# Kernel optimization log

Measured on AMD Instinct MI355X. Metric: run time of the kernel, lower is better.

Reference implementation:

```python
import jax, jax.numpy as jnp
import numpy as np

T, B, D = 512, 64, 1024


def setup_inputs() -> dict:
    key = jax.random.key(0)
    k1, k2, k3, k4 = jax.random.split(key, 4)
    scale = 1.0 / np.sqrt(D)
    x = jax.random.normal(k1, (T, B, D), dtype=jnp.float32)
    resets = jax.random.randint(k2, (T, B), 0, 2) > 0  # bool reset mask per step
    Wi = jax.random.normal(k3, (D, 3 * D), dtype=jnp.float32) * scale  # [ir|iz|in]
    bi = jnp.zeros((3 * D,), dtype=jnp.float32)
    Wh = jax.random.normal(k4, (D, 3 * D), dtype=jnp.float32) * scale  # [hr|hz|hn]
    bhn = jnp.zeros((D,), dtype=jnp.float32)  # bias only on hn gate (flax GRUCell)
    return {"x": x, "Wi": Wi, "bi": bi, "Wh": Wh, "bhn": bhn, "resets": resets}


def reference(x, Wi, bi, Wh, bhn, resets):
    """Scan of flax nn.GRUCell with reset-masked carry. x: [T,B,D], resets: [T,B] bool."""
    Bsz, Dh = x.shape[1], x.shape[2]

    def step(h, inp):
        xt, rt = inp  # xt: [B,D], rt: [B]
        h = jnp.where(rt[:, None], jnp.zeros_like(h), h)  # reset carry to zeros
        gi = xt @ Wi + bi          # [B,3D]
        gh = h @ Wh                # [B,3D] (no bias for r,z in flax GRUCell)
        ir_, iz_, in_ = jnp.split(gi, 3, axis=-1)
        hr_, hz_, hn_ = jnp.split(gh, 3, axis=-1)
        r = jax.nn.sigmoid(ir_ + hr_)
        z = jax.nn.sigmoid(iz_ + hz_)
        n = jnp.tanh(in_ + r * (hn_ + bhn))
        h_new = (1.0 - z) * n + z * h
        return h_new, h_new

    h0 = jnp.zeros((Bsz, Dh), dtype=x.dtype)  # flax initialize_carry default: zeros
    _, ys = jax.lax.scan(step, h0, (x, resets))
    return ys  # [T,B,D]
```

## Files before the change

### kernel.cpp

```cpp
#include <hip/hip_runtime.h>


typedef __attribute__((ext_vector_type(8))) short short8;
typedef __attribute__((ext_vector_type(4))) float f32x4;
typedef __attribute__((ext_vector_type(4))) unsigned int u32x4;

#define DEV static __device__ __forceinline__

constexpr int TT = 512, BB = 64, DD = 1024, TD = 3072;

constexpr size_t WS_BAR = 256;
constexpr size_t WS_H = 8192;
constexpr size_t HPLANE = (size_t)BB * DD * 2;
constexpr size_t WS_NEED = WS_H + 4 * HPLANE;

DEV unsigned short f2bf(float f) {
    unsigned u = __builtin_bit_cast(unsigned, f);
    u += 0x7FFFu + ((u >> 16) & 1u);
    return (unsigned short)(u >> 16);
}
DEV float bf2f(unsigned short s) { return __builtin_bit_cast(float, ((unsigned)s) << 16); }

DEV void ld16_sc1(u32x4& r, const unsigned* p) {
    asm volatile("global_load_dwordx4 %0, %1, off sc1" : "=v"(r) : "v"(p));
}
DEV void ld16(u32x4& r, const unsigned* p) {
    asm volatile("global_load_dwordx4 %0, %1, off" : "=v"(r) : "v"(p));
}
DEV void ld8u(unsigned& r, const unsigned char* p) {
    asm volatile("global_load_ubyte %0, %1, off" : "=v"(r) : "v"(p));
}
DEV void st16_sc1(unsigned short* p, unsigned v) {
    asm volatile("global_store_short %0, %1, off sc1" :: "v"(p), "v"(v) : "memory");
}
DEV void coh_store_u32(unsigned* p, unsigned v) {
    asm volatile("global_store_dword %0, %1, off sc1" :: "v"(p), "v"(v) : "memory");
}
DEV void vm0() {
    asm volatile("s_waitcnt vmcnt(0)" ::: "memory");
    __builtin_amdgcn_sched_barrier(0);
}

__global__ void pack_x_kernel(const float* __restrict__ x, unsigned* __restrict__ outw) {
    const size_t gid = (size_t)blockIdx.x * 256 + threadIdx.x;
    const size_t e0 = gid * 8;
    const unsigned t = (unsigned)(e0 >> 16);
    const unsigned p = (unsigned)(e0 & 65535u);
    f32x4 a = *(const f32x4*)(x + e0);
    f32x4 b = *(const f32x4*)(x + e0 + 4);
    u32x4 wh, wl;
#pragma unroll
    for (int j = 0; j < 2; ++j) {
        unsigned short h0 = f2bf(a[2 * j]), h1 = f2bf(a[2 * j + 1]);
        wh[j] = (unsigned)h0 | ((unsigned)h1 << 16);
        wl[j] = (unsigned)f2bf(a[2 * j] - bf2f(h0)) | ((unsigned)f2bf(a[2 * j + 1] - bf2f(h1)) << 16);
        unsigned short g0 = f2bf(b[2 * j]), g1 = f2bf(b[2 * j + 1]);
        wh[2 + j] = (unsigned)g0 | ((unsigned)g1 << 16);
        wl[2 + j] = (unsigned)f2bf(b[2 * j] - bf2f(g0)) | ((unsigned)f2bf(b[2 * j + 1] - bf2f(g1)) << 16);
    }
    unsigned* base = outw + (size_t)t * 65536u;
    *(u32x4*)(base + (p >> 1)) = wh;
    *(u32x4*)(base + 32768u + (p >> 1)) = wl;
}

__global__ void prep_kernel(const unsigned char* __restrict__ resets, unsigned char* __restrict__ ws) {
    const int bid = blockIdx.x, tid = threadIdx.x;
    if (bid < 256) {
        ((unsigned*)(ws + WS_H))[bid * 256 + tid] = 0u;
    } else {
        unsigned* w32 = (unsigned*)ws;
        for (int i = tid; i < 2048; i += 256) w32[i] = 0u;
        __shared__ int ca, cb, cc;
        if (tid == 0) { ca = 0; cb = 0; cc = 0; }
        __syncthreads();
        int la = 0, lb = 0, lc = 0;
        for (int o = tid * 16; o < tid * 16 + 16; ++o) {
            unsigned char v = resets[o];
            if (v) {
                if ((o & 3) == 0) la = 1; else lb = 1;
                if ((o & 7) == 4) lc = 1;
            }
        }
        if (la) atomicOr(&ca, 1);
        if (lb) atomicOr(&cb, 1);
        if (lc) atomicOr(&cc, 1);
        __syncthreads();
        if (tid == 0) {
            unsigned stride, boff = 0;
            if (ca && cb)       { stride = 1; }
            else if (!ca && cb) { stride = 4; boff = 3; }
            else if (ca && cc)  { stride = 4; }
            else if (ca)        { stride = 8; }
            else                { stride = 4; }
            w32[0] = stride; w32[1] = boff;
        }
    }
}

DEV void arrive_epoch(unsigned* bar, int grp, unsigned ep) {
    unsigned old = __hip_atomic_fetch_add(&bar[grp * 32], 1u, __ATOMIC_RELAXED, __HIP_MEMORY_SCOPE_AGENT);
    if (old == ep * 16u - 1u) {
        unsigned oldr = __hip_atomic_fetch_add(&bar[512], 1u, __ATOMIC_RELAXED, __HIP_MEMORY_SCOPE_AGENT);
        if (oldr == ep * 16u - 1u) {
#pragma unroll
            for (int g = 0; g < 16; ++g) coh_store_u32(&bar[544 + g * 32], ep);
            asm volatile("s_waitcnt vmcnt(0)" ::: "memory");
        }
    }
}
DEV void wait_epoch(unsigned* bar, int grp, unsigned ep) {
    while (__hip_atomic_load(&bar[544 + grp * 32], __ATOMIC_RELAXED, __HIP_MEMORY_SCOPE_AGENT) < ep) {}
}

__launch_bounds__(512, 1)
__global__ void gru_kernel(const float* __restrict__ Wi, const float* __restrict__ bi,
                           const float* __restrict__ Wh, const float* __restrict__ bhn,
                           const unsigned char* __restrict__ resets,
                           float* __restrict__ out, unsigned char* __restrict__ ws) {
    const int tid = threadIdx.x;
    const int wg = blockIdx.x;
    const int lane = tid & 63;
    const int kw = tid >> 6;
    const int mgrp = wg >> 6;
    const int c0 = (wg & 63) * 16;
    const int grp = wg >> 4;

    unsigned* bar = (unsigned*)(ws + WS_BAR);
    const unsigned rstride = ((const unsigned*)ws)[0];
    const unsigned rboff   = ((const unsigned*)ws)[1];

    unsigned short* h_hi[2] = {(unsigned short*)(ws + WS_H),
                               (unsigned short*)(ws + WS_H + 2 * HPLANE)};
    unsigned short* h_lo[2] = {(unsigned short*)(ws + WS_H + HPLANE),
                               (unsigned short*)(ws + WS_H + 3 * HPLANE)};
    unsigned* outw = (unsigned*)out;

    const int lrow = lane & 15;
    const int lk = (lane >> 4) * 8;

    short8 bih[3][4], bhh[3][4], bhl[3][4];
#pragma unroll
    for (int nt = 0; nt < 3; ++nt) {
        const int col = nt * DD + c0 + lrow;
#pragma unroll
        for (int kt = 0; kt < 4; ++kt) {
            const int kb = kw * 128 + kt * 32 + lk;
            short8 a, c, d;
#pragma unroll
            for (int j = 0; j < 8; ++j) {
                float wi = Wi[(size_t)(kb + j) * TD + col];
                a[j] = (short)f2bf(wi);
                float wh = Wh[(size_t)(kb + j) * TD + col];
                unsigned short h2 = f2bf(wh);
                c[j] = (short)h2;
                d[j] = (short)f2bf(wh - bf2f(h2));
            }
            bih[nt][kt] = a; bhh[nt][kt] = c; bhl[nt][kt] = d;
        }
    }

    const int eb = (tid & 255) >> 4, ej = tid & 15;
    const int brow = mgrp * 16 + eb;
    const int ce = c0 + ej;
    const float bi_r = bi[ce], bi_z = bi[DD + ce], bi_n = bi[2 * DD + ce];
    const float bh_n = bhn[ce];
    float h_local = 0.f;

    const int arow = mgrp * 16 + lrow;
    const unsigned hidx = (unsigned)(arow * DD + kw * 128 + lk);
    const size_t r64 = (size_t)64 * rstride;
    const size_t roffb = (size_t)brow * rstride + rboff;

    __shared__ float pgi[8][3][16][18];
    __shared__ float pgh[8][3][16][18];
    const int prow = (lane >> 4) * 4;

    {
        const unsigned* xpl = outw;
        u32x4 xf[8];
#pragma unroll
        for (int kt = 0; kt < 4; ++kt) {
            ld16(xf[2 * kt],     xpl + ((hidx + kt * 32) >> 1));
            ld16(xf[2 * kt + 1], xpl + 32768u + ((hidx + kt * 32) >> 1));
        }
        vm0();
        f32x4 ai[3] = {f32x4{0}, f32x4{0}, f32x4{0}};
#pragma unroll
        for (int kt = 0; kt < 4; ++kt) {
            short8 xh = __builtin_bit_cast(short8, xf[2 * kt]);
            short8 xl = __builtin_bit_cast(short8, xf[2 * kt + 1]);
#pragma unroll
            for (int nt = 0; nt < 3; ++nt)
                ai[nt] = __builtin_amdgcn_mfma_f32_16x16x32_bf16(xh, bih[nt][kt], ai[nt], 0, 0, 0);
#pragma unroll
            for (int nt = 0; nt < 3; ++nt)
                ai[nt] = __builtin_amdgcn_mfma_f32_16x16x32_bf16(xl, bih[nt][kt], ai[nt], 0, 0, 0);
        }
#pragma unroll
        for (int s = 0; s < 3; ++s)
#pragma unroll
            for (int i = 0; i < 4; ++i)
                pgi[kw][s][prow + i][lrow] = ai[s][i];
        __syncthreads();
        if (tid == 0) arrive_epoch(bar, grp, 1u);
    }

    int cur = 0;
    for (int t = 0; t < TT - 1; ++t) {
        if (tid == 0) wait_epoch(bar, grp, (unsigned)(t + 1));
        __syncthreads();

        const unsigned* hhp = (const unsigned*)h_hi[cur];
        const unsigned* hlp = (const unsigned*)h_lo[cur];
        u32x4 hf[8];
#pragma unroll
        for (int kt = 0; kt < 4; ++kt) {
            ld16_sc1(hf[2 * kt],     hhp + ((hidx + kt * 32) >> 1));
            ld16_sc1(hf[2 * kt + 1], hlp + ((hidx + kt * 32) >> 1));
        }

        float g0 = 0.f, g1 = 0.f, g2 = 0.f;
        if (tid < 256) {
#pragma unroll
            for (int k = 0; k < 8; ++k) {
                g0 += pgi[k][0][eb][ej];
                g1 += pgi[k][1][eb][ej];
                g2 += pgi[k][2][eb][ej];
            }
        }

        vm0();

        const unsigned* xpl = outw + (size_t)(t + 1) * 65536u;
        u32x4 xf[8];
#pragma unroll
        for (int kt = 0; kt < 4; ++kt) {
            ld16(xf[2 * kt],     xpl + ((hidx + kt * 32) >> 1));
            ld16(xf[2 * kt + 1], xpl + 32768u + ((hidx + kt * 32) >> 1));
        }
        unsigned rsv;
        ld8u(rsv, resets + roffb + (size_t)(t + 1) * r64);

        f32x4 ag[3] = {f32x4{0}, f32x4{0}, f32x4{0}};
#pragma unroll
        for (int kt = 0; kt < 4; ++kt) {
            short8 hh = __builtin_bit_cast(short8, hf[2 * kt]);
            short8 hl = __builtin_bit_cast(short8, hf[2 * kt + 1]);
#pragma unroll
            for (int nt = 0; nt < 3; ++nt)
                ag[nt] = __builtin_amdgcn_mfma_f32_16x16x32_bf16(hh, bhh[nt][kt], ag[nt], 0, 0, 0);
#pragma unroll
            for (int nt = 0; nt < 3; ++nt)
                ag[nt] = __builtin_amdgcn_mfma_f32_16x16x32_bf16(hl, bhh[nt][kt], ag[nt], 0, 0, 0);
#pragma unroll
            for (int nt = 0; nt < 3; ++nt)
                ag[nt] = __builtin_amdgcn_mfma_f32_16x16x32_bf16(hh, bhl[nt][kt], ag[nt], 0, 0, 0);
        }

#pragma unroll
        for (int s = 0; s < 3; ++s)
#pragma unroll
            for (int i = 0; i < 4; ++i)
                pgh[kw][s][prow + i][lrow] = ag[s][i];
        __syncthreads();

        vm0();

        f32x4 ai[3] = {f32x4{0}, f32x4{0}, f32x4{0}};
#pragma unroll
        for (int kt = 0; kt < 4; ++kt) {
            short8 xh = __builtin_bit_cast(short8, xf[2 * kt]);
            short8 xl = __builtin_bit_cast(short8, xf[2 * kt + 1]);
#pragma unroll
            for (int nt = 0; nt < 3; ++nt)
                ai[nt] = __builtin_amdgcn_mfma_f32_16x16x32_bf16(xh, bih[nt][kt], ai[nt], 0, 0, 0);
#pragma unroll
            for (int nt = 0; nt < 3; ++nt)
                ai[nt] = __builtin_amdgcn_mfma_f32_16x16x32_bf16(xl, bih[nt][kt], ai[nt], 0, 0, 0);
        }
#pragma unroll
        for (int s = 0; s < 3; ++s)
#pragma unroll
            for (int i = 0; i < 4; ++i)
                pgi[kw][s][prow + i][lrow] = ai[s][i];

        if (tid < 256) {
            float h0 = 0.f, h1 = 0.f, h2 = 0.f;
#pragma unroll
            for (int k = 0; k < 8; ++k) {
                h0 += pgh[k][0][eb][ej];
                h1 += pgh[k][1][eb][ej];
                h2 += pgh[k][2][eb][ej];
            }
            float r = 1.f / (1.f + __expf(-(g0 + bi_r + h0)));
            float z = 1.f / (1.f + __expf(-(g1 + bi_z + h1)));
            float pre = g2 + bi_n + r * (h2 + bh_n);
            float e2 = __expf(2.f * pre);
            float n = 1.f - 2.f / (e2 + 1.f);
            float hnew = (1.f - z) * n + z * h_local;

            out[(size_t)t * 65536u + brow * DD + ce] = hnew;

            float heff = (rsv != 0u) ? 0.f : hnew;
            h_local = heff;
            unsigned short ph = f2bf(heff);
            unsigned short pl = f2bf(heff - bf2f(ph));
            st16_sc1(h_hi[cur ^ 1] + brow * DD + ce, (unsigned)ph);
            st16_sc1(h_lo[cur ^ 1] + brow * DD + ce, (unsigned)pl);
        }

        asm volatile("s_waitcnt vmcnt(0)" ::: "memory");
        __syncthreads();
        if (tid == 0) arrive_epoch(bar, grp, (unsigned)(t + 2));
        cur ^= 1;
    }

    {
        const int t = TT - 1;
        if (tid == 0) wait_epoch(bar, grp, (unsigned)TT);
        __syncthreads();

        const unsigned* hhp = (const unsigned*)h_hi[cur];
        const unsigned* hlp = (const unsigned*)h_lo[cur];
        u32x4 hf[8];
#pragma unroll
        for (int kt = 0; kt < 4; ++kt) {
            ld16_sc1(hf[2 * kt],     hhp + ((hidx + kt * 32) >> 1));
            ld16_sc1(hf[2 * kt + 1], hlp + ((hidx + kt * 32) >> 1));
        }
        float g0 = 0.f, g1 = 0.f, g2 = 0.f;
        if (tid < 256) {
#pragma unroll
            for (int k = 0; k < 8; ++k) {
                g0 += pgi[k][0][eb][ej];
                g1 += pgi[k][1][eb][ej];
                g2 += pgi[k][2][eb][ej];
            }
        }
        vm0();
        f32x4 ag[3] = {f32x4{0}, f32x4{0}, f32x4{0}};
#pragma unroll
        for (int kt = 0; kt < 4; ++kt) {
            short8 hh = __builtin_bit_cast(short8, hf[2 * kt]);
            short8 hl = __builtin_bit_cast(short8, hf[2 * kt + 1]);
#pragma unroll
            for (int nt = 0; nt < 3; ++nt)
                ag[nt] = __builtin_amdgcn_mfma_f32_16x16x32_bf16(hh, bhh[nt][kt], ag[nt], 0, 0, 0);
#pragma unroll
            for (int nt = 0; nt < 3; ++nt)
                ag[nt] = __builtin_amdgcn_mfma_f32_16x16x32_bf16(hl, bhh[nt][kt], ag[nt], 0, 0, 0);
#pragma unroll
            for (int nt = 0; nt < 3; ++nt)
                ag[nt] = __builtin_amdgcn_mfma_f32_16x16x32_bf16(hh, bhl[nt][kt], ag[nt], 0, 0, 0);
        }
#pragma unroll
        for (int s = 0; s < 3; ++s)
#pragma unroll
            for (int i = 0; i < 4; ++i)
                pgh[kw][s][prow + i][lrow] = ag[s][i];
        __syncthreads();

        if (tid < 256) {
            float h0 = 0.f, h1 = 0.f, h2 = 0.f;
#pragma unroll
            for (int k = 0; k < 8; ++k) {
                h0 += pgh[k][0][eb][ej];
                h1 += pgh[k][1][eb][ej];
                h2 += pgh[k][2][eb][ej];
            }
            float r = 1.f / (1.f + __expf(-(g0 + bi_r + h0)));
            float z = 1.f / (1.f + __expf(-(g1 + bi_z + h1)));
            float pre = g2 + bi_n + r * (h2 + bh_n);
            float e2 = __expf(2.f * pre);
            float n = 1.f - 2.f / (e2 + 1.f);
            float hnew = (1.f - z) * n + z * h_local;
            out[(size_t)t * 65536u + brow * DD + ce] = hnew;
        }
    }
}

extern "C" void kernel_launch(void* const* d_in, const int* in_sizes, int n_in,
                              void* d_out, int out_size, void* d_ws, size_t ws_size,
                              hipStream_t stream) {
    const float* x = (const float*)d_in[0];
    const float* Wi = (const float*)d_in[1];
    const float* bi = (const float*)d_in[2];
    const float* Wh = (const float*)d_in[3];
    const float* bhn = (const float*)d_in[4];
    const unsigned char* resets = (const unsigned char*)d_in[5];
    float* out = (float*)d_out;
    unsigned char* ws = (unsigned char*)d_ws;

    if (ws_size < WS_NEED) return;

    hipLaunchKernelGGL(pack_x_kernel, dim3(16384), dim3(256), 0, stream, x, (unsigned*)out);
    hipLaunchKernelGGL(prep_kernel, dim3(257), dim3(256), 0, stream, resets, ws);

    void* args[] = {(void*)&Wi, (void*)&bi, (void*)&Wh, (void*)&bhn,
                    (void*)&resets, (void*)&out, (void*)&ws};
    hipError_t err = hipLaunchCooperativeKernel((const void*)gru_kernel, dim3(256), dim3(512),
                                                args, 0, stream);
    if (err != hipSuccess) {
        hipLaunchKernelGGL(gru_kernel, dim3(256), dim3(512), 0, stream,
                           Wi, bi, Wh, bhn, resets, out, ws);
    }
}
```

Baseline: 2.947 ms.

## Use per-batch-group counter barrier and move x projection off critical path

Replaces the global two-level epoch barrier with per-batch-group counters: 64 workgroups share eight sub-counters, and waiters poll and sum them. The x input projection for the next step now runs after the workgroup arrives at the barrier, overlapping it with other workgroups' progress. Packed x is re-laid out so each batch group's slice is contiguous, and output stores are deferred by one step. This shortens the serial per-timestep critical path, at the cost of more polling loads and a bounded spin guard that could exit early if the guard runs out.

```diff
diff --git a/kernel.cpp b/kernel.cpp
--- a/kernel.cpp
+++ b/kernel.cpp
@@ -4,6 +4,7 @@
 typedef __attribute__((ext_vector_type(8))) short short8;
 typedef __attribute__((ext_vector_type(4))) float f32x4;
 typedef __attribute__((ext_vector_type(4))) unsigned int u32x4;
+typedef __attribute__((ext_vector_type(2))) unsigned long long u64x2;
 
 #define DEV static __device__ __forceinline__
 
@@ -21,20 +22,11 @@
 }
 DEV float bf2f(unsigned short s) { return __builtin_bit_cast(float, ((unsigned)s) << 16); }
 
-DEV void ld16_sc1(u32x4& r, const unsigned* p) {
-    asm volatile("global_load_dwordx4 %0, %1, off sc1" : "=v"(r) : "v"(p));
-}
 DEV void ld16(u32x4& r, const unsigned* p) {
     asm volatile("global_load_dwordx4 %0, %1, off" : "=v"(r) : "v"(p));
 }
 DEV void ld8u(unsigned& r, const unsigned char* p) {
     asm volatile("global_load_ubyte %0, %1, off" : "=v"(r) : "v"(p));
-}
-DEV void st16_sc1(unsigned short* p, unsigned v) {
-    asm volatile("global_store_short %0, %1, off sc1" :: "v"(p), "v"(v) : "memory");
-}
-DEV void coh_store_u32(unsigned* p, unsigned v) {
-    asm volatile("global_store_dword %0, %1, off sc1" :: "v"(p), "v"(v) : "memory");
 }
 DEV void vm0() {
     asm volatile("s_waitcnt vmcnt(0)" ::: "memory");
@@ -46,6 +38,8 @@
     const size_t e0 = gid * 8;
     const unsigned t = (unsigned)(e0 >> 16);
     const unsigned p = (unsigned)(e0 & 65535u);
+    const unsigned r = p >> 10, d = p & 1023u;
+    const unsigned m = r >> 4, lr = r & 15u;
     f32x4 a = *(const f32x4*)(x + e0);
     f32x4 b = *(const f32x4*)(x + e0 + 4);
     u32x4 wh, wl;
@@ -58,9 +52,9 @@
         wh[2 + j] = (unsigned)g0 | ((unsigned)g1 << 16);
         wl[2 + j] = (unsigned)f2bf(b[2 * j] - bf2f(g0)) | ((unsigned)f2bf(b[2 * j + 1] - bf2f(g1)) << 16);
     }
-    unsigned* base = outw + (size_t)t * 65536u;
-    *(u32x4*)(base + (p >> 1)) = wh;
-    *(u32x4*)(base + 32768u + (p >> 1)) = wl;
+    unsigned* base = outw + (size_t)t * 65536u + m * 16384u + ((lr * 1024u + d) >> 1);
+    *(u32x4*)base = wh;
+    *(u32x4*)(base + 8192u) = wl;
 }
 
 __global__ void prep_kernel(const unsigned char* __restrict__ resets, unsigned char* __restrict__ ws) {
@@ -95,21 +89,6 @@
             w32[0] = stride; w32[1] = boff;
         }
     }
-}
-
-DEV void arrive_epoch(unsigned* bar, int grp, unsigned ep) {
-    unsigned old = __hip_atomic_fetch_add(&bar[grp * 32], 1u, __ATOMIC_RELAXED, __HIP_MEMORY_SCOPE_AGENT);
-    if (old == ep * 16u - 1u) {
-        unsigned oldr = __hip_atomic_fetch_add(&bar[512], 1u, __ATOMIC_RELAXED, __HIP_MEMORY_SCOPE_AGENT);
-        if (oldr == ep * 16u - 1u) {
-#pragma unroll
-            for (int g = 0; g < 16; ++g) coh_store_u32(&bar[544 + g * 32], ep);
-            asm volatile("s_waitcnt vmcnt(0)" ::: "memory");
-        }
-    }
-}
-DEV void wait_epoch(unsigned* bar, int grp, unsigned ep) {
-    while (__hip_atomic_load(&bar[544 + grp * 32], __ATOMIC_RELAXED, __HIP_MEMORY_SCOPE_AGENT) < ep) {}
 }
 
 __launch_bounds__(512, 1)
@@ -122,10 +101,11 @@
     const int lane = tid & 63;
     const int kw = tid >> 6;
     const int mgrp = wg >> 6;
-    const int c0 = (wg & 63) * 16;
-    const int grp = wg >> 4;
-
-    unsigned* bar = (unsigned*)(ws + WS_BAR);
+    const int cg = wg & 63;
+    const int c0 = cg * 16;
+
+    unsigned* bar = (unsigned*)(ws + WS_BAR) + mgrp * 256;
+    unsigned* rep = &bar[(cg & 7) * 32];
     const unsigned rstride = ((const unsigned*)ws)[0];
     const unsigned rboff   = ((const unsigned*)ws)[1];
 
@@ -165,9 +145,11 @@
     const float bi_r = bi[ce], bi_z = bi[DD + ce], bi_n = bi[2 * DD + ce];
     const float bh_n = bhn[ce];
     float h_local = 0.f;
-
-    const int arow = mgrp * 16 + lrow;
-    const unsigned hidx = (unsigned)(arow * DD + kw * 128 + lk);
+    float ys_prev = 0.f;
+
+    const unsigned xlidx = (unsigned)(lrow * 1024 + kw * 128 + lk);
+    const unsigned xwbase = (unsigned)mgrp * 16384u + (xlidx >> 1);
+    const unsigned hidx = (unsigned)((mgrp * 16 + lrow) * 1024 + kw * 128 + lk);
     const size_t r64 = (size_t)64 * rstride;
     const size_t roffb = (size_t)brow * rstride + rboff;
 
@@ -175,14 +157,17 @@
     __shared__ float pgh[8][3][16][18];
     const int prow = (lane >> 4) * 4;
 
+    unsigned rsv = 0;
+
     {
         const unsigned* xpl = outw;
         u32x4 xf[8];
 #pragma unroll
         for (int kt = 0; kt < 4; ++kt) {
-            ld16(xf[2 * kt],     xpl + ((hidx + kt * 32) >> 1));
-            ld16(xf[2 * kt + 1], xpl + 32768u + ((hidx + kt * 32) >> 1));
-        }
+            ld16(xf[2 * kt],     xpl + xwbase + kt * 16);
+            ld16(xf[2 * kt + 1], xpl + xwbase + 8192u + kt * 16);
+        }
+        ld8u(rsv, resets + roffb + r64);
         vm0();
         f32x4 ai[3] = {f32x4{0}, f32x4{0}, f32x4{0}};
 #pragma unroll
@@ -201,22 +186,33 @@
 #pragma unroll
             for (int i = 0; i < 4; ++i)
                 pgi[kw][s][prow + i][lrow] = ai[s][i];
-        __syncthreads();
-        if (tid == 0) arrive_epoch(bar, grp, 1u);
-    }
-
-    int cur = 0;
-    for (int t = 0; t < TT - 1; ++t) {
-        if (tid == 0) wait_epoch(bar, grp, (unsigned)(t + 1));
-        __syncthreads();
-
-        const unsigned* hhp = (const unsigned*)h_hi[cur];
-        const unsigned* hlp = (const unsigned*)h_lo[cur];
-        u32x4 hf[8];
-#pragma unroll
-        for (int kt = 0; kt < 4; ++kt) {
-            ld16_sc1(hf[2 * kt],     hhp + ((hidx + kt * 32) >> 1));
-            ld16_sc1(hf[2 * kt + 1], hlp + ((hidx + kt * 32) >> 1));
+    }
+
+    for (int t = 0; t < TT; ++t) {
+        if (tid == 0 && t) {
+            const unsigned target = 64u * (unsigned)t;
+            int guard = 1 << 20;
+            unsigned s;
+            do {
+                s = 0;
+#pragma unroll
+                for (int r2 = 0; r2 < 8; ++r2)
+                    s += __hip_atomic_load(&bar[r2 * 32], __ATOMIC_RELAXED, __HIP_MEMORY_SCOPE_AGENT);
+            } while (s < target && --guard);
+        }
+        __syncthreads();
+
+        const int cur = t & 1;
+        const unsigned long long* hh64 = (const unsigned long long*)h_hi[cur];
+        const unsigned long long* hl64 = (const unsigned long long*)h_lo[cur];
+        unsigned long long vh[8], vl[8];
+#pragma unroll
+        for (int kt = 0; kt < 4; ++kt) {
+            const unsigned b = (hidx + kt * 32) >> 2;
+            vh[2 * kt]     = __hip_atomic_load(hh64 + b,     __ATOMIC_RELAXED, __HIP_MEMORY_SCOPE_AGENT);
+            vh[2 * kt + 1] = __hip_atomic_load(hh64 + b + 1, __ATOMIC_RELAXED, __HIP_MEMORY_SCOPE_AGENT);
+            vl[2 * kt]     = __hip_atomic_load(hl64 + b,     __ATOMIC_RELAXED, __HIP_MEMORY_SCOPE_AGENT);
+            vl[2 * kt + 1] = __hip_atomic_load(hl64 + b + 1, __ATOMIC_RELAXED, __HIP_MEMORY_SCOPE_AGENT);
         }
 
         float g0 = 0.f, g1 = 0.f, g2 = 0.f;
@@ -229,32 +225,20 @@
             }
         }
 
-        vm0();
-
-        const unsigned* xpl = outw + (size_t)(t + 1) * 65536u;
-        u32x4 xf[8];
-#pragma unroll
-        for (int kt = 0; kt < 4; ++kt) {
-            ld16(xf[2 * kt],     xpl + ((hidx + kt * 32) >> 1));
-            ld16(xf[2 * kt + 1], xpl + 32768u + ((hidx + kt * 32) >> 1));
-        }
-        unsigned rsv;
-        ld8u(rsv, resets + roffb + (size_t)(t + 1) * r64);
-
         f32x4 ag[3] = {f32x4{0}, f32x4{0}, f32x4{0}};
 #pragma unroll
         for (int kt = 0; kt < 4; ++kt) {
-            short8 hh = __builtin_bit_cast(short8, hf[2 * kt]);
-            short8 hl = __builtin_bit_cast(short8, hf[2 * kt + 1]);
-#pragma unroll
-            for (int nt = 0; nt < 3; ++nt)
+            u64x2 a1, a2;
+            a1[0] = vh[2 * kt]; a1[1] = vh[2 * kt + 1];
+            a2[0] = vl[2 * kt]; a2[1] = vl[2 * kt + 1];
+            short8 hh = __builtin_bit_cast(short8, a1);
+            short8 hl = __builtin_bit_cast(short8, a2);
+#pragma unroll
+            for (int nt = 0; nt < 3; ++nt) {
                 ag[nt] = __builtin_amdgcn_mfma_f32_16x16x32_bf16(hh, bhh[nt][kt], ag[nt], 0, 0, 0);
-#pragma unroll
-            for (int nt = 0; nt < 3; ++nt)
                 ag[nt] = __builtin_amdgcn_mfma_f32_16x16x32_bf16(hl, bhh[nt][kt], ag[nt], 0, 0, 0);
-#pragma unroll
-            for (int nt = 0; nt < 3; ++nt)
                 ag[nt] = __builtin_amdgcn_mfma_f32_16x16x32_bf16(hh, bhl[nt][kt], ag[nt], 0, 0, 0);
+            }
         }
 
 #pragma unroll
@@ -263,26 +247,6 @@
             for (int i = 0; i < 4; ++i)
                 pgh[kw][s][prow + i][lrow] = ag[s][i];
         __syncthreads();
-
-        vm0();
-
-        f32x4 ai[3] = {f32x4{0}, f32x4{0}, f32x4{0}};
-#pragma unroll
-        for (int kt = 0; kt < 4; ++kt) {
-            short8 xh = __builtin_bit_cast(short8, xf[2 * kt]);
-            short8 xl = __builtin_bit_cast(short8, xf[2 * kt + 1]);
-#pragma unroll
-            for (int nt = 0; nt < 3; ++nt)
-                ai[nt] = __builtin_amdgcn_mfma_f32_16x16x32_bf16(xh, bih[nt][kt], ai[nt], 0, 0, 0);
-#pragma unroll
-            for (int nt = 0; nt < 3; ++nt)
-                ai[nt] = __builtin_amdgcn_mfma_f32_16x16x32_bf16(xl, bih[nt][kt], ai[nt], 0, 0, 0);
-        }
-#pragma unroll
-        for (int s = 0; s < 3; ++s)
-#pragma unroll
-            for (int i = 0; i < 4; ++i)
-                pgi[kw][s][prow + i][lrow] = ai[s][i];
 
         if (tid < 256) {
             float h0 = 0.f, h1 = 0.f, h2 = 0.f;
@@ -299,84 +263,60 @@
             float n = 1.f - 2.f / (e2 + 1.f);
             float hnew = (1.f - z) * n + z * h_local;
 
-            out[(size_t)t * 65536u + brow * DD + ce] = hnew;
-
-            float heff = (rsv != 0u) ? 0.f : hnew;
-            h_local = heff;
-            unsigned short ph = f2bf(heff);
-            unsigned short pl = f2bf(heff - bf2f(ph));
-            st16_sc1(h_hi[cur ^ 1] + brow * DD + ce, (unsigned)ph);
-            st16_sc1(h_lo[cur ^ 1] + brow * DD + ce, (unsigned)pl);
+            if (t) out[(size_t)(t - 1) * 65536u + brow * DD + ce] = ys_prev;
+            ys_prev = hnew;
+
+            if (t < TT - 1) {
+                float heff = (rsv != 0u) ? 0.f : hnew;
+                h_local = heff;
+                unsigned short ph = f2bf(heff);
+                unsigned short pl = f2bf(heff - bf2f(ph));
+                __hip_atomic_store(h_hi[cur ^ 1] + brow * DD + ce, ph,
+                                   __ATOMIC_RELAXED, __HIP_MEMORY_SCOPE_AGENT);
+                __hip_atomic_store(h_lo[cur ^ 1] + brow * DD + ce, pl,
+                                   __ATOMIC_RELAXED, __HIP_MEMORY_SCOPE_AGENT);
+            }
         }
 
         asm volatile("s_waitcnt vmcnt(0)" ::: "memory");
         __syncthreads();
-        if (tid == 0) arrive_epoch(bar, grp, (unsigned)(t + 2));
-        cur ^= 1;
-    }
-
-    {
-        const int t = TT - 1;
-        if (tid == 0) wait_epoch(bar, grp, (unsigned)TT);
-        __syncthreads();
-
-        const unsigned* hhp = (const unsigned*)h_hi[cur];
-        const unsigned* hlp = (const unsigned*)h_lo[cur];
-        u32x4 hf[8];
-#pragma unroll
-        for (int kt = 0; kt < 4; ++kt) {
-            ld16_sc1(hf[2 * kt],     hhp + ((hidx + kt * 32) >> 1));
-            ld16_sc1(hf[2 * kt + 1], hlp + ((hidx + kt * 32) >> 1));
-        }
-        float g0 = 0.f, g1 = 0.f, g2 = 0.f;
-        if (tid < 256) {
-#pragma unroll
-            for (int k = 0; k < 8; ++k) {
-                g0 += pgi[k][0][eb][ej];
-                g1 += pgi[k][1][eb][ej];
-                g2 += pgi[k][2][eb][ej];
-            }
-        }
-        vm0();
-        f32x4 ag[3] = {f32x4{0}, f32x4{0}, f32x4{0}};
-#pragma unroll
-        for (int kt = 0; kt < 4; ++kt) {
-            short8 hh = __builtin_bit_cast(short8, hf[2 * kt]);
-            short8 hl = __builtin_bit_cast(short8, hf[2 * kt + 1]);
-#pragma unroll
-            for (int nt = 0; nt < 3; ++nt)
-                ag[nt] = __builtin_amdgcn_mfma_f32_16x16x32_bf16(hh, bhh[nt][kt], ag[nt], 0, 0, 0);
-#pragma unroll
-            for (int nt = 0; nt < 3; ++nt)
-                ag[nt] = __builtin_amdgcn_mfma_f32_16x16x32_bf16(hl, bhh[nt][kt], ag[nt], 0, 0, 0);
-#pragma unroll
-            for (int nt = 0; nt < 3; ++nt)
-                ag[nt] = __builtin_amdgcn_mfma_f32_16x16x32_bf16(hh, bhl[nt][kt], ag[nt], 0, 0, 0);
-        }
-#pragma unroll
-        for (int s = 0; s < 3; ++s)
-#pragma unroll
-            for (int i = 0; i < 4; ++i)
-                pgh[kw][s][prow + i][lrow] = ag[s][i];
-        __syncthreads();
-
-        if (tid < 256) {
-            float h0 = 0.f, h1 = 0.f, h2 = 0.f;
-#pragma unroll
-            for (int k = 0; k < 8; ++k) {
-                h0 += pgh[k][0][eb][ej];
-                h1 += pgh[k][1][eb][ej];
-                h2 += pgh[k][2][eb][ej];
-            }
-            float r = 1.f / (1.f + __expf(-(g0 + bi_r + h0)));
-            float z = 1.f / (1.f + __expf(-(g1 + bi_z + h1)));
-            float pre = g2 + bi_n + r * (h2 + bh_n);
-            float e2 = __expf(2.f * pre);
-            float n = 1.f - 2.f / (e2 + 1.f);
-            float hnew = (1.f - z) * n + z * h_local;
-            out[(size_t)t * 65536u + brow * DD + ce] = hnew;
-        }
-    }
+
+        if (t < TT - 1) {
+            if (tid == 0)
+                __hip_atomic_fetch_add(rep, 1u, __ATOMIC_RELAXED, __HIP_MEMORY_SCOPE_AGENT);
+
+            const unsigned* xpl = outw + (size_t)(t + 1) * 65536u;
+            u32x4 xf[8];
+#pragma unroll
+            for (int kt = 0; kt < 4; ++kt) {
+                ld16(xf[2 * kt],     xpl + xwbase + kt * 16);
+                ld16(xf[2 * kt + 1], xpl + xwbase + 8192u + kt * 16);
+            }
+            const int ridx = (t + 2 < TT) ? (t + 2) : (TT - 1);
+            ld8u(rsv, resets + roffb + (size_t)ridx * r64);
+            vm0();
+            f32x4 ai[3] = {f32x4{0}, f32x4{0}, f32x4{0}};
+#pragma unroll
+            for (int kt = 0; kt < 4; ++kt) {
+                short8 xh = __builtin_bit_cast(short8, xf[2 * kt]);
+                short8 xl = __builtin_bit_cast(short8, xf[2 * kt + 1]);
+#pragma unroll
+                for (int nt = 0; nt < 3; ++nt)
+                    ai[nt] = __builtin_amdgcn_mfma_f32_16x16x32_bf16(xh, bih[nt][kt], ai[nt], 0, 0, 0);
+#pragma unroll
+                for (int nt = 0; nt < 3; ++nt)
+                    ai[nt] = __builtin_amdgcn_mfma_f32_16x16x32_bf16(xl, bih[nt][kt], ai[nt], 0, 0, 0);
+            }
+#pragma unroll
+            for (int s = 0; s < 3; ++s)
+#pragma unroll
+                for (int i = 0; i < 4; ++i)
+                    pgi[kw][s][prow + i][lrow] = ai[s][i];
+        }
+    }
+
+    if (tid < 256)
+        out[(size_t)(TT - 1) * 65536u + brow * DD + ce] = ys_prev;
 }
 
 extern "C" void kernel_launch(void* const* d_in, const int* in_sizes, int n_in,
```

Result: slower. 3.895 ms (+32.1%).
